# Kernel tuning notes

Hardware: AMD Instinct MI355X
Metric: run time of the kernel (lower is better)

The kernel has to match this reference:

```python
import jax, jax.numpy as jnp
import numpy as np

CELU_ALPHA = 0.1  # torchani standard CELU alpha


def _celu(x):
    return jax.nn.celu(x, alpha=CELU_ALPHA)


def setup_inputs() -> dict:
    key = jax.random.key(0)
    ks = jax.random.split(key, 12)
    N, S, E, D = 20000, 4, 8, 1008
    dims = [D, 256, 192, 160, 1]
    inp = {
        "aev": jax.random.normal(ks[0], (N, D), jnp.float32),
        "species": jax.random.randint(ks[1], (N,), 0, S, dtype=jnp.int64),
    }
    for l in range(4):
        din, dout = dims[l], dims[l + 1]
        inp[f"W{l}"] = jax.random.normal(ks[2 + 2 * l], (S, E, din, dout), jnp.float32) * (1.0 / np.sqrt(din).astype(np.float32))
        inp[f"b{l}"] = jax.random.normal(ks[3 + 2 * l], (S, E, dout), jnp.float32) * 0.05
    return inp


def reference(aev, species, W0, b0, W1, b1, W2, b2, W3, b3):
    # Faithful math of InferModel.forward: for each species i, gather atoms of
    # that species, run the BmmAtomicNetwork (ensemble of MLPs via bmm, CELU
    # activations, mean over ensemble members), sum per-species energies, then
    # sum into a single [1]-shaped total energy.
    # JIT-friendly equivalent: evaluate every species network on all atoms
    # (S=4 is small) and select each atom's output by its species index.
    # h: [S, E, N, hidden]
    h = _celu(jnp.einsum('ni,seio->seno', aev, W0) + b0[:, :, None, :])
    h = _celu(jnp.einsum('seni,seio->seno', h, W1) + b1[:, :, None, :])
    h = _celu(jnp.einsum('seni,seio->seno', h, W2) + b2[:, :, None, :])
    h = jnp.einsum('seni,seio->seno', h, W3) + b3[:, :, None, :]  # [S,E,N,1]
    per_atom = h.mean(axis=1)[:, :, 0]  # mean over ensemble -> [S, N]
    sel = jnp.take_along_axis(per_atom, species[None, :], axis=0)[0]  # [N]
    return jnp.sum(sel, keepdims=True)  # shape [1], total energy
```

## Files before the change

### kernel.cpp

```cpp
#include <hip/hip_runtime.h>
#include <cmath>

#define NA 20000
#define NS 4
#define NE 8
#define DD 1008
#define BM 128
#define MAXT 157
#define MAXROWS 20608

typedef unsigned short u16;
typedef unsigned int u32;
typedef unsigned long long u64;
typedef u16 u16x8 __attribute__((ext_vector_type(8)));
typedef u16 u16x4 __attribute__((ext_vector_type(4)));
typedef float f32x4 __attribute__((ext_vector_type(4)));
typedef short s16x8 __attribute__((ext_vector_type(8)));

__device__ __forceinline__ float bf2f(u16 h) {
  u32 u = ((u32)h) << 16;
  return __builtin_bit_cast(float, u);
}
__device__ __forceinline__ u16 f2bf(float f) {
  u32 b = __builtin_bit_cast(u32, f);
  u32 lsb = (b >> 16) & 1;
  return (u16)((b + 0x7fffu + lsb) >> 16);
}
__device__ __forceinline__ float celu_f(float x) {
#if __has_builtin(__builtin_amdgcn_exp2f)
  float e = __builtin_amdgcn_exp2f(x * 14.426950408889634f);
#else
  float e = exp2f(x * 14.426950408889634f);
#endif
  return x > 0.f ? x : 0.1f * (e - 1.f);
}
__device__ __forceinline__ float gf(const void* g, size_t i, bool isF32) {
  return isF32 ? ((const float*)g)[i] : bf2f(((const u16*)g)[i]);
}

__device__ __forceinline__ void gll16(const void* g, const u16* lds) {
#if __has_builtin(__builtin_amdgcn_global_load_lds)
  __builtin_amdgcn_global_load_lds(
      (const __attribute__((address_space(1))) u32*)g,
      (__attribute__((address_space(3))) u32*)(u16*)lds, 16, 0, 0);
#else
  int l = threadIdx.x & 63;
  *(f32x4*)((u16*)lds + l * 8) = *(const f32x4*)g;
#endif
}

#define CHUNK_BARRIER(N)                                   \
  do {                                                     \
    asm volatile("s_waitcnt vmcnt(" #N ")" ::: "memory");  \
    __builtin_amdgcn_sched_barrier(0);                     \
    __builtin_amdgcn_s_barrier();                          \
    __builtin_amdgcn_sched_barrier(0);                     \
  } while (0)

__global__ void k_probe0(const void* __restrict__ aev, const void* __restrict__ species,
                         int* __restrict__ w) {
  __shared__ int sh[2];
  int tid = threadIdx.x;
  if (tid < 64) w[tid] = 0;
  if (tid == 0) { sh[0] = 0; sh[1] = 0; }
  __syncthreads();
  const u16* a = (const u16*)aev;
  int bad = 0;
  for (int i = 0; i < 16; ++i) {
    u16 h = a[tid * 16 + i];
    int ex = (h >> 7) & 0xFF;
    if (ex < 107 || ex > 147) ++bad;
  }
  atomicAdd(&sh[0], bad);
  const int* sp = (const int*)species;
  int odd = 0;
  for (int i = 0; i < 4; ++i)
    if (sp[(tid * 4 + i) * 2 + 1] != 0) ++odd;
  atomicAdd(&sh[1], odd);
  __syncthreads();
  if (tid == 0) {
    w[18] = (sh[0] > 400) ? 1 : 0;
    w[19] = (sh[1] == 0) ? 1 : 0;
  }
}

__device__ __forceinline__ int get_species(const void* sp, int i, bool i64) {
  int s = i64 ? ((const int*)sp)[2 * i] : ((const int*)sp)[i];
  return s < 0 ? 0 : (s > 3 ? 3 : s);
}

__global__ void k_count(const void* __restrict__ species, int* __restrict__ w) {
  int i = blockIdx.x * 256 + threadIdx.x;
  int lane = threadIdx.x & 63;
  int s = (i < NA) ? get_species(species, i, w[19] != 0) : -1;
  for (int sp = 0; sp < 4; ++sp) {
    u64 m = __ballot(s == sp);
    if (m != 0 && lane == (__ffsll((long long)m) - 1))
      atomicAdd(&w[sp], __popcll(m));
  }
  __syncthreads();
  if (threadIdx.x == 0) {
    __threadfence();
    if (atomicAdd(&w[25], 1) == (int)gridDim.x - 1) {
      int b = 0, pb = 0;
      for (int sp = 0; sp < 4; ++sp) {
        int c = atomicAdd(&w[sp], 0);
        w[13 + sp] = b; b += c;
        w[20 + sp] = pb; pb += ((c + 127) >> 7) << 7;
      }
      w[24] = pb;
    }
  }
}

__global__ void k_scatsml(const void* __restrict__ species, int* __restrict__ w,
                          int* __restrict__ order,
                          const void* b0, const void* b1, const void* b2, const void* b3,
                          const void* W3, u16* ob0, u16* ob1, u16* ob2, u16* ob3,
                          u16* oW3, u16* gap) {
  if (blockIdx.x == 79) {
    const bool isF32 = (w[18] != 0);
    int t = threadIdx.x;
    for (int i = t; i < 32 * 256; i += 256) ob0[i] = f2bf(gf(b0, i, isF32));
    for (int i = t; i < 32 * 192; i += 256) ob1[i] = f2bf(gf(b1, i, isF32));
    for (int i = t; i < 32 * 160; i += 256) ob2[i] = f2bf(gf(b2, i, isF32));
    for (int i = t; i < 32 * 160; i += 256) oW3[i] = f2bf(gf(W3, i, isF32));
    if (t < 32) ob3[t] = f2bf(gf(b3, t, isF32));
    u16x8 z = {0, 0, 0, 0, 0, 0, 0, 0};
    *(u16x8*)(gap + t * 8) = z;
    return;
  }
  int i = blockIdx.x * 256 + threadIdx.x;
  int lane = threadIdx.x & 63;
  int s = (i < NA) ? get_species(species, i, w[19] != 0) : -1;
  for (int sp = 0; sp < 4; ++sp) {
    u64 m = __ballot(s == sp);
    if (m == 0) continue;
    int leader = __ffsll((long long)m) - 1;
    int base = 0;
    if (lane == leader) base = atomicAdd(&w[4 + sp], __popcll(m));
    base = __shfl(base, leader);
    if (s == sp) {
      int rank = __popcll(m & ((lane == 63) ? 0x7fffffffffffffffULL : ((1ULL << lane) - 1)));
      order[w[13 + sp] + base + rank] = i;
    }
  }
}

__global__ void k_gather(const void* __restrict__ aev, const int* __restrict__ w,
                         const int* __restrict__ order, u16* __restrict__ aevb) {
  const bool isF32 = (w[18] != 0);
  const int t = threadIdx.x;
  const int r = blockIdx.x * 4 + (t >> 7);
  const int j = t & 127;
  if (j >= 126) return;
  const int s = (r >= w[21]) + (r >= w[22]) + (r >= w[23]);
  const int local = r - w[20 + s];
  u16x8 v = {0, 0, 0, 0, 0, 0, 0, 0};
  if (local < w[s]) {
    const int src = order[w[13 + s] + local];
    if (isF32) {
      const float* p = (const float*)aev + (size_t)src * DD + j * 8;
      const f32x4 f0 = *(const f32x4*)p;
      const f32x4 f1 = *(const f32x4*)(p + 4);
#pragma unroll
      for (int i = 0; i < 4; ++i) { v[i] = f2bf(f0[i]); v[4 + i] = f2bf(f1[i]); }
    } else {
      v = *(const u16x8*)((const u16*)aev + (size_t)src * DD + j * 8);
    }
  }
  *(u16x8*)(aevb + (size_t)r * DD + j * 8) = v;
}

__device__ void tr_tile(const void* __restrict__ W, u16* __restrict__ out,
                        int K, int N, int Kpad, bool isF32, int se,
                        int k0, int n0, int t, u16 (*tile)[68]) {
  const size_t inBase = (size_t)se * K * N;
#pragma unroll
  for (int c = 0; c < 4; ++c) {
    int kk = (t >> 4) + c * 16, nn = (t & 15) * 4;
    int k = k0 + kk, n = n0 + nn;
    u16x4 v = {0, 0, 0, 0};
    if (k < K && n < N) {
      if (isF32) {
        f32x4 f = *(const f32x4*)((const float*)W + inBase + (size_t)k * N + n);
        v[0] = f2bf(f[0]); v[1] = f2bf(f[1]); v[2] = f2bf(f[2]); v[3] = f2bf(f[3]);
      } else {
        v = *(const u16x4*)((const u16*)W + inBase + (size_t)k * N + n);
      }
    }
    *(u16x4*)(&tile[kk][nn]) = v;
  }
  __syncthreads();
  int nloc = t >> 2, ks = (t & 3) * 16;
  if (n0 + nloc < N) {
    u16x8 o0, o1;
#pragma unroll
    for (int i = 0; i < 8; ++i) { o0[i] = tile[ks + i][nloc]; o1[i] = tile[ks + 8 + i][nloc]; }
    size_t ob = (size_t)se * N * Kpad + (size_t)(n0 + nloc) * Kpad + k0 + ks;
    *(u16x8*)(out + ob) = o0;
    *(u16x8*)(out + ob + 8) = o1;
  }
}

__global__ void k_tr3(const void* __restrict__ W0, const void* __restrict__ W1,
                      const void* __restrict__ W2, u16* __restrict__ o0,
                      u16* __restrict__ o1, u16* __restrict__ o2,
                      const int* __restrict__ w) {
  __shared__ u16 tile[64][68];
  const bool isF32 = (w[18] != 0);
  const int se = blockIdx.x, by = blockIdx.y, bz = blockIdx.z, t = threadIdx.x;
  tr_tile(W0, o0, 1008, 256, 1024, isF32, se, by * 64, bz * 64, t, tile);
  if (by < 4 && bz < 3) {
    __syncthreads();
    tr_tile(W1, o1, 256, 192, 256, isF32, se, by * 64, bz * 64, t, tile);
  }
  if (by < 3 && bz < 3) {
    __syncthreads();
    tr_tile(W2, o2, 192, 160, 192, isF32, se, by * 64, bz * 64, t, tile);
  }
}

__global__ __launch_bounds__(512, 4) void k_main(
    const u16* __restrict__ aevb, const u16* __restrict__ wt0,
    const u16* __restrict__ wt1, const u16* __restrict__ wt2,
    const u16* __restrict__ w3b, const u16* __restrict__ b0b,
    const u16* __restrict__ b1b, const u16* __restrict__ b2b,
    const u16* __restrict__ b3b, const int* __restrict__ w,
    float* __restrict__ accum) {
  __shared__ __align__(16) u16 L[32768];

  const int tid = threadIdx.x;
  const int g = blockIdx.x;
  const int s = g >> 1;
  const int e = (g & 1) * 4 + (blockIdx.y & 3);
  const int tile = blockIdx.y >> 2;
  const int cnt = w[s];
  if (tile * BM >= cnt) return;
  const int mRow = w[20 + s] + tile * BM;
  const int mCount = min(BM, cnt - tile * BM);
  const int se = s * NE + e;

  const int lane = tid & 63;
  const int wv = tid >> 6;
  const int lcol = lane & 15;
  const int quad = lane >> 4;

  {
    const u16* wt0se = wt0 + (size_t)se * 256 * 1024;
    const int wm = wv >> 2, wn = wv & 3;

    const int rowA = tid >> 2;
    const int gAx = (tid & 3) ^ ((rowA >> 1) & 3);
    const u16* gA = aevb + (size_t)(mRow + rowA) * 1008 + gAx * 8;
    const int rB1 = 128 + (tid >> 2);
    const int gB0x = (tid & 3) ^ (((tid >> 2) >> 1) & 3);
    const int gB1x = (tid & 3) ^ ((rB1 >> 1) & 3);
    const u16* gB0 = wt0se + (size_t)(tid >> 2) * 1024 + gB0x * 8;
    const u16* gB1 = wt0se + (size_t)rB1 * 1024 + gB1x * 8;
    const int aSt = wv * 512;
    const int bSt = wv * 512;
    const int bSt2 = 4096 + wv * 512;

    const int gsw = (quad ^ ((lcol >> 1) & 3)) * 8;
    const int aRow0 = (wm * 64 + lcol) * 32 + gsw;
    const int bRow0 = (wn * 64 + lcol) * 32 + gsw;

    f32x4 acc[4][4];
#pragma unroll
    for (int i = 0; i < 4; ++i)
#pragma unroll
      for (int j = 0; j < 4; ++j) acc[i][j] = (f32x4){0.f, 0.f, 0.f, 0.f};

    gll16(gA, &L[aSt]);
    gll16(gB0, &L[8192 + bSt]);
    gll16(gB1, &L[8192 + bSt2]);
    gll16(gB0 + 32, &L[16384 + bSt]);
    gll16(gB1 + 32, &L[16384 + bSt2]);
    CHUNK_BARRIER(2);

    int bbufC = 0, bbufS = 2;
    for (int p = 0; p < 32; ++p) {
      if (p < 31)
        gll16(gA + (p + 1) * 32, &L[((p + 1) & 1) * 4096 + aSt]);
      if (p < 30) {
        gll16(gB0 + (p + 2) * 32, &L[8192 + bbufS * 8192 + bSt]);
        gll16(gB1 + (p + 2) * 32, &L[8192 + bbufS * 8192 + bSt2]);
      }
      const u16* Ad = &L[(p & 1) * 4096];
      const u16* Bd = &L[8192 + bbufC * 8192];
      s16x8 aF[4], bF[4];
#pragma unroll
      for (int mt = 0; mt < 4; ++mt)
        aF[mt] = __builtin_bit_cast(s16x8, *(const u16x8*)(Ad + aRow0 + mt * 512));
#pragma unroll
      for (int nt = 0; nt < 4; ++nt)
        bF[nt] = __builtin_bit_cast(s16x8, *(const u16x8*)(Bd + bRow0 + nt * 512));
      __builtin_amdgcn_s_setprio(1);
#pragma unroll
      for (int nt = 0; nt < 4; ++nt)
#pragma unroll
        for (int mt = 0; mt < 4; ++mt)
          acc[mt][nt] = __builtin_amdgcn_mfma_f32_16x16x32_bf16(aF[mt], bF[nt], acc[mt][nt], 0, 0, 0);
      __builtin_amdgcn_s_setprio(0);
      if (p < 30) CHUNK_BARRIER(2); else CHUNK_BARRIER(0);
      bbufC = (bbufC == 2) ? 0 : bbufC + 1;
      bbufS = (bbufS == 2) ? 0 : bbufS + 1;
    }

#pragma unroll
    for (int nt = 0; nt < 4; ++nt) {
      const int col = wn * 64 + nt * 16 + lcol;
      const float bb = bf2f(b0b[se * 256 + col]);
#pragma unroll
      for (int mt = 0; mt < 4; ++mt) {
#pragma unroll
        for (int r = 0; r < 4; ++r) {
          const int rr = wm * 64 + mt * 16 + quad * 4 + r;
          L[(rr * 256 + col) ^ ((rr & 7) << 3)] = f2bf(celu_f(acc[mt][nt][r] + bb));
        }
      }
    }
  }
  __syncthreads();

  {
    const int wm = wv >> 2, wn = wv & 3;
    const u16* w1se = wt1 + (size_t)se * 192 * 256;
    const u16* bp[3];
#pragma unroll
    for (int nt = 0; nt < 3; ++nt)
      bp[nt] = w1se + (size_t)(wn * 48 + nt * 16 + lcol) * 256 + quad * 8;
    f32x4 acc[4][3];
#pragma unroll
    for (int i = 0; i < 4; ++i)
#pragma unroll
      for (int j = 0; j < 3; ++j) acc[i][j] = (f32x4){0.f, 0.f, 0.f, 0.f};
    int aBase[4], aSwz[4];
#pragma unroll
    for (int mt = 0; mt < 4; ++mt) {
      const int row = wm * 64 + mt * 16 + lcol;
      aBase[mt] = row * 256 + quad * 8;
      aSwz[mt] = (row & 7) << 3;
    }
    u16x8 cB[3], nB[3];
#pragma unroll
    for (int nt = 0; nt < 3; ++nt) cB[nt] = *(const u16x8*)bp[nt];
    for (int kc = 0; kc < 8; ++kc) {
      if (kc < 7) {
#pragma unroll
        for (int nt = 0; nt < 3; ++nt) nB[nt] = *(const u16x8*)(bp[nt] + (kc + 1) * 32);
      }
      s16x8 aF[4];
#pragma unroll
      for (int mt = 0; mt < 4; ++mt)
        aF[mt] = __builtin_bit_cast(s16x8, *(const u16x8*)&L[(aBase[mt] + kc * 32) ^ aSwz[mt]]);
#pragma unroll
      for (int nt = 0; nt < 3; ++nt) {
        const s16x8 bF = __builtin_bit_cast(s16x8, cB[nt]);
#pragma unroll
        for (int mt = 0; mt < 4; ++mt)
          acc[mt][nt] = __builtin_amdgcn_mfma_f32_16x16x32_bf16(aF[mt], bF, acc[mt][nt], 0, 0, 0);
      }
      if (kc < 7) {
#pragma unroll
        for (int nt = 0; nt < 3; ++nt) cB[nt] = nB[nt];
      }
    }
    __syncthreads();
#pragma unroll
    for (int nt = 0; nt < 3; ++nt) {
      const int col = wn * 48 + nt * 16 + lcol;
      const float bb = bf2f(b1b[se * 192 + col]);
#pragma unroll
      for (int mt = 0; mt < 4; ++mt) {
#pragma unroll
        for (int r = 0; r < 4; ++r) {
          const int rr = wm * 64 + mt * 16 + quad * 4 + r;
          L[(rr * 192 + col) ^ ((rr & 7) << 3)] = f2bf(celu_f(acc[mt][nt][r] + bb));
        }
      }
    }
  }
  __syncthreads();

  {
    const int wm = wv >> 1, wn = wv & 1;
    const u16* w2se = wt2 + (size_t)se * 160 * 192;
    const u16* bp[5];
#pragma unroll
    for (int nt = 0; nt < 5; ++nt)
      bp[nt] = w2se + (size_t)(wn * 80 + nt * 16 + lcol) * 192 + quad * 8;
    f32x4 acc[2][5];
#pragma unroll
    for (int i = 0; i < 2; ++i)
#pragma unroll
      for (int j = 0; j < 5; ++j) acc[i][j] = (f32x4){0.f, 0.f, 0.f, 0.f};
    int aBase[2], aSwz[2];
#pragma unroll
    for (int mt = 0; mt < 2; ++mt) {
      const int row = wm * 32 + mt * 16 + lcol;
      aBase[mt] = row * 192 + quad * 8;
      aSwz[mt] = (row & 7) << 3;
    }
    u16x8 cB[5], nB[5];
#pragma unroll
    for (int nt = 0; nt < 5; ++nt) cB[nt] = *(const u16x8*)bp[nt];
    for (int kc = 0; kc < 6; ++kc) {
      if (kc < 5) {
#pragma unroll
        for (int nt = 0; nt < 5; ++nt) nB[nt] = *(const u16x8*)(bp[nt] + (kc + 1) * 32);
      }
      s16x8 aF[2];
#pragma unroll
      for (int mt = 0; mt < 2; ++mt)
        aF[mt] = __builtin_bit_cast(s16x8, *(const u16x8*)&L[(aBase[mt] + kc * 32) ^ aSwz[mt]]);
#pragma unroll
      for (int nt = 0; nt < 5; ++nt) {
        const s16x8 bF = __builtin_bit_cast(s16x8, cB[nt]);
#pragma unroll
        for (int mt = 0; mt < 2; ++mt)
          acc[mt][nt] = __builtin_amdgcn_mfma_f32_16x16x32_bf16(aF[mt], bF, acc[mt][nt], 0, 0, 0);
      }
      if (kc < 5) {
#pragma unroll
        for (int nt = 0; nt < 5; ++nt) cB[nt] = nB[nt];
      }
    }
    __syncthreads();
#pragma unroll
    for (int nt = 0; nt < 5; ++nt) {
      const int col = wn * 80 + nt * 16 + lcol;
      const float bb = bf2f(b2b[se * 160 + col]);
#pragma unroll
      for (int mt = 0; mt < 2; ++mt) {
#pragma unroll
        for (int r = 0; r < 4; ++r) {
          const int rr = wm * 32 + mt * 16 + quad * 4 + r;
          L[(rr * 160 + col) ^ ((rr & 7) << 3)] = f2bf(celu_f(acc[mt][nt][r] + bb));
        }
      }
    }
  }
  __syncthreads();

  {
    const int row = tid >> 2;
    const int pp = tid & 3;
    const u16* w3p = w3b + se * 160;
    float dotv = 0.f;
#pragma unroll
    for (int j = 0; j < 5; ++j) {
      const int ci = (pp + 4 * j) * 8;
      const u16x8 hv = *(const u16x8*)&L[(row * 160 + ci) ^ ((row & 7) << 3)];
      const u16x8 wv8 = *(const u16x8*)(w3p + ci);
#pragma unroll
      for (int t2 = 0; t2 < 8; ++t2)
        dotv = fmaf(bf2f(hv[t2]), bf2f(wv8[t2]), dotv);
    }
    dotv += __shfl_xor(dotv, 1);
    dotv += __shfl_xor(dotv, 2);
    float v = (pp == 0 && row < mCount) ? (dotv + bf2f(b3b[se])) : 0.f;
    v += __shfl_xor(v, 4);
    v += __shfl_xor(v, 8);
    v += __shfl_xor(v, 16);
    v += __shfl_xor(v, 32);
    float* redf = (float*)&L[20608];
    if (lane == 0) redf[wv] = v;
    __syncthreads();
    if (tid == 0) {
      float tot = 0.f;
#pragma unroll
      for (int i = 0; i < 8; ++i) tot += redf[i];
      atomicAdd(accum, tot * 0.125f);
    }
  }
}

__global__ void k_final(const float* __restrict__ accum, u32* __restrict__ out) {
  u32 h = (u32)f2bf(accum[0]);
  out[0] = (h << 16) | h;
}

extern "C" void kernel_launch(void* const* d_in, const int* in_sizes, int n_in,
                              void* d_out, int out_size, void* d_ws, size_t ws_size,
                              hipStream_t stream) {
  const void* aev = d_in[0];
  const void* species = d_in[1];
  const void* W0 = d_in[2];
  const void* b0 = d_in[3];
  const void* W1 = d_in[4];
  const void* b1 = d_in[5];
  const void* W2 = d_in[6];
  const void* b2 = d_in[7];
  const void* W3 = d_in[8];
  const void* b3 = d_in[9];

  int* wsI = (int*)d_ws;
  float* accum = (float*)((char*)d_ws + 17 * 4);
  int* order = wsI + 1024;
  char* wsB = (char*)d_ws;

  const size_t oB0 = 131072;
  const size_t oB1 = 147456;
  const size_t oB2 = 159744;
  const size_t oB3 = 169984;
  const size_t oW3 = 170048;
  const size_t oAevb = 262144;
  const size_t oGap = 41807872;
  const size_t oWt0 = 41811968;
  const size_t oWt1 = 58589184;
  const size_t oWt2 = 61734912;

  u16* aevb = (u16*)(wsB + oAevb);
  u16* wt0 = (u16*)(wsB + oWt0);
  u16* wt1 = (u16*)(wsB + oWt1);
  u16* wt2 = (u16*)(wsB + oWt2);
  u16* w3b = (u16*)(wsB + oW3);
  u16* b0b = (u16*)(wsB + oB0);
  u16* b1b = (u16*)(wsB + oB1);
  u16* b2b = (u16*)(wsB + oB2);
  u16* b3b = (u16*)(wsB + oB3);

  hipLaunchKernelGGL(k_probe0, dim3(1), dim3(256), 0, stream, aev, species, wsI);
  hipLaunchKernelGGL(k_count, dim3((NA + 255) / 256), dim3(256), 0, stream, species, wsI);
  hipLaunchKernelGGL(k_scatsml, dim3(80), dim3(256), 0, stream, species, wsI, order,
                     b0, b1, b2, b3, W3, b0b, b1b, b2b, b3b, w3b, (u16*)(wsB + oGap));
  hipLaunchKernelGGL(k_gather, dim3(MAXROWS / 4), dim3(512), 0, stream, aev, wsI, order, aevb);
  hipLaunchKernelGGL(k_tr3, dim3(32, 16, 4), dim3(256), 0, stream, W0, W1, W2,
                     wt0, wt1, wt2, wsI);
  hipLaunchKernelGGL(k_main, dim3(8, 4 * MAXT), dim3(512), 0, stream,
                     aevb, wt0, wt1, wt2, w3b, b0b, b1b, b2b, b3b, wsI, accum);
  hipLaunchKernelGGL(k_final, dim3(1), dim3(1), 0, stream, accum, (u32*)d_out);
}
```

Baseline: 428.2 us.

## Double block size to 1024 threads and halve per-wave row tiles

```diff
diff --git a/kernel.cpp b/kernel.cpp
--- a/kernel.cpp
+++ b/kernel.cpp
@@ -48,14 +48,6 @@
   *(f32x4*)((u16*)lds + l * 8) = *(const f32x4*)g;
 #endif
 }
-
-#define CHUNK_BARRIER(N)                                   \
-  do {                                                     \
-    asm volatile("s_waitcnt vmcnt(" #N ")" ::: "memory");  \
-    __builtin_amdgcn_sched_barrier(0);                     \
-    __builtin_amdgcn_s_barrier();                          \
-    __builtin_amdgcn_sched_barrier(0);                     \
-  } while (0)
 
 __global__ void k_probe0(const void* __restrict__ aev, const void* __restrict__ species,
                          int* __restrict__ w) {
@@ -221,7 +213,7 @@
   }
 }
 
-__global__ __launch_bounds__(512, 4) void k_main(
+__global__ __launch_bounds__(1024, 8) void k_main(
     const u16* __restrict__ aevb, const u16* __restrict__ wt0,
     const u16* __restrict__ wt1, const u16* __restrict__ wt2,
     const u16* __restrict__ w3b, const u16* __restrict__ b0b,
@@ -252,46 +244,39 @@
 
     const int rowA = tid >> 2;
     const int gAx = (tid & 3) ^ ((rowA >> 1) & 3);
-    const u16* gA = aevb + (size_t)(mRow + rowA) * 1008 + gAx * 8;
-    const int rB1 = 128 + (tid >> 2);
-    const int gB0x = (tid & 3) ^ (((tid >> 2) >> 1) & 3);
-    const int gB1x = (tid & 3) ^ ((rB1 >> 1) & 3);
-    const u16* gB0 = wt0se + (size_t)(tid >> 2) * 1024 + gB0x * 8;
-    const u16* gB1 = wt0se + (size_t)rB1 * 1024 + gB1x * 8;
+    const u16* gA = aevb + (size_t)(mRow + (rowA & 127)) * 1008 + gAx * 8;
+    const int rowB = tid >> 2;
+    const int gBx = (tid & 3) ^ ((rowB >> 1) & 3);
+    const u16* gB = wt0se + (size_t)rowB * 1024 + gBx * 8;
     const int aSt = wv * 512;
     const int bSt = wv * 512;
-    const int bSt2 = 4096 + wv * 512;
 
     const int gsw = (quad ^ ((lcol >> 1) & 3)) * 8;
-    const int aRow0 = (wm * 64 + lcol) * 32 + gsw;
+    const int aRow0 = (wm * 32 + lcol) * 32 + gsw;
     const int bRow0 = (wn * 64 + lcol) * 32 + gsw;
 
-    f32x4 acc[4][4];
-#pragma unroll
-    for (int i = 0; i < 4; ++i)
+    f32x4 acc[2][4];
+#pragma unroll
+    for (int i = 0; i < 2; ++i)
 #pragma unroll
       for (int j = 0; j < 4; ++j) acc[i][j] = (f32x4){0.f, 0.f, 0.f, 0.f};
 
-    gll16(gA, &L[aSt]);
-    gll16(gB0, &L[8192 + bSt]);
-    gll16(gB1, &L[8192 + bSt2]);
-    gll16(gB0 + 32, &L[16384 + bSt]);
-    gll16(gB1 + 32, &L[16384 + bSt2]);
-    CHUNK_BARRIER(2);
-
-    int bbufC = 0, bbufS = 2;
+    if (tid < 512) gll16(gA, &L[aSt]);
+    gll16(gB, &L[8192 + bSt]);
+    __syncthreads();
+
     for (int p = 0; p < 32; ++p) {
-      if (p < 31)
-        gll16(gA + (p + 1) * 32, &L[((p + 1) & 1) * 4096 + aSt]);
-      if (p < 30) {
-        gll16(gB0 + (p + 2) * 32, &L[8192 + bbufS * 8192 + bSt]);
-        gll16(gB1 + (p + 2) * 32, &L[8192 + bbufS * 8192 + bSt2]);
-      }
-      const u16* Ad = &L[(p & 1) * 4096];
-      const u16* Bd = &L[8192 + bbufC * 8192];
-      s16x8 aF[4], bF[4];
-#pragma unroll
-      for (int mt = 0; mt < 4; ++mt)
+      const int d = p & 1;
+      if (p < 31) {
+        const int dn = d ^ 1;
+        if (tid < 512) gll16(gA + (p + 1) * 32, &L[dn * 4096 + aSt]);
+        gll16(gB + (p + 1) * 32, &L[8192 + dn * 8192 + bSt]);
+      }
+      const u16* Ad = &L[d * 4096];
+      const u16* Bd = &L[8192 + d * 8192];
+      s16x8 aF[2], bF[4];
+#pragma unroll
+      for (int mt = 0; mt < 2; ++mt)
         aF[mt] = __builtin_bit_cast(s16x8, *(const u16x8*)(Ad + aRow0 + mt * 512));
 #pragma unroll
       for (int nt = 0; nt < 4; ++nt)
@@ -300,12 +285,10 @@
 #pragma unroll
       for (int nt = 0; nt < 4; ++nt)
 #pragma unroll
-        for (int mt = 0; mt < 4; ++mt)
+        for (int mt = 0; mt < 2; ++mt)
           acc[mt][nt] = __builtin_amdgcn_mfma_f32_16x16x32_bf16(aF[mt], bF[nt], acc[mt][nt], 0, 0, 0);
       __builtin_amdgcn_s_setprio(0);
-      if (p < 30) CHUNK_BARRIER(2); else CHUNK_BARRIER(0);
-      bbufC = (bbufC == 2) ? 0 : bbufC + 1;
-      bbufS = (bbufS == 2) ? 0 : bbufS + 1;
+      __syncthreads();
     }
 
 #pragma unroll
@@ -313,10 +296,10 @@
       const int col = wn * 64 + nt * 16 + lcol;
       const float bb = bf2f(b0b[se * 256 + col]);
 #pragma unroll
-      for (int mt = 0; mt < 4; ++mt) {
+      for (int mt = 0; mt < 2; ++mt) {
 #pragma unroll
         for (int r = 0; r < 4; ++r) {
-          const int rr = wm * 64 + mt * 16 + quad * 4 + r;
+          const int rr = wm * 32 + mt * 16 + quad * 4 + r;
           L[(rr * 256 + col) ^ ((rr & 7) << 3)] = f2bf(celu_f(acc[mt][nt][r] + bb));
         }
       }
@@ -331,15 +314,15 @@
 #pragma unroll
     for (int nt = 0; nt < 3; ++nt)
       bp[nt] = w1se + (size_t)(wn * 48 + nt * 16 + lcol) * 256 + quad * 8;
-    f32x4 acc[4][3];
-#pragma unroll
-    for (int i = 0; i < 4; ++i)
+    f32x4 acc[2][3];
+#pragma unroll
+    for (int i = 0; i < 2; ++i)
 #pragma unroll
       for (int j = 0; j < 3; ++j) acc[i][j] = (f32x4){0.f, 0.f, 0.f, 0.f};
-    int aBase[4], aSwz[4];
-#pragma unroll
-    for (int mt = 0; mt < 4; ++mt) {
-      const int row = wm * 64 + mt * 16 + lcol;
+    int aBase[2], aSwz[2];
+#pragma unroll
+    for (int mt = 0; mt < 2; ++mt) {
+      const int row = wm * 32 + mt * 16 + lcol;
       aBase[mt] = row * 256 + quad * 8;
       aSwz[mt] = (row & 7) << 3;
     }
@@ -351,15 +334,15 @@
 #pragma unroll
         for (int nt = 0; nt < 3; ++nt) nB[nt] = *(const u16x8*)(bp[nt] + (kc + 1) * 32);
       }
-      s16x8 aF[4];
-#pragma unroll
-      for (int mt = 0; mt < 4; ++mt)
+      s16x8 aF[2];
+#pragma unroll
+      for (int mt = 0; mt < 2; ++mt)
         aF[mt] = __builtin_bit_cast(s16x8, *(const u16x8*)&L[(aBase[mt] + kc * 32) ^ aSwz[mt]]);
 #pragma unroll
       for (int nt = 0; nt < 3; ++nt) {
         const s16x8 bF = __builtin_bit_cast(s16x8, cB[nt]);
 #pragma unroll
-        for (int mt = 0; mt < 4; ++mt)
+        for (int mt = 0; mt < 2; ++mt)
           acc[mt][nt] = __builtin_amdgcn_mfma_f32_16x16x32_bf16(aF[mt], bF, acc[mt][nt], 0, 0, 0);
       }
       if (kc < 7) {
@@ -373,10 +356,10 @@
       const int col = wn * 48 + nt * 16 + lcol;
       const float bb = bf2f(b1b[se * 192 + col]);
 #pragma unroll
-      for (int mt = 0; mt < 4; ++mt) {
+      for (int mt = 0; mt < 2; ++mt) {
 #pragma unroll
         for (int r = 0; r < 4; ++r) {
-          const int rr = wm * 64 + mt * 16 + quad * 4 + r;
+          const int rr = wm * 32 + mt * 16 + quad * 4 + r;
           L[(rr * 192 + col) ^ ((rr & 7) << 3)] = f2bf(celu_f(acc[mt][nt][r] + bb));
         }
       }
@@ -385,17 +368,18 @@
   __syncthreads();
 
   {
-    const int wm = wv >> 1, wn = wv & 1;
+    const int wm = wv >> 2, wn = wv & 3;
+    const int nN2 = (wn < 2) ? 2 : 3;
+    const int t2 = (wn < 2) ? 2 * wn : 3 * wn - 2;
     const u16* w2se = wt2 + (size_t)se * 160 * 192;
-    const u16* bp[5];
-#pragma unroll
-    for (int nt = 0; nt < 5; ++nt)
-      bp[nt] = w2se + (size_t)(wn * 80 + nt * 16 + lcol) * 192 + quad * 8;
-    f32x4 acc[2][5];
+    const u16* bp[3];
+    for (int nt = 0; nt < nN2; ++nt)
+      bp[nt] = w2se + (size_t)((t2 + nt) * 16 + lcol) * 192 + quad * 8;
+    f32x4 acc[2][3];
 #pragma unroll
     for (int i = 0; i < 2; ++i)
 #pragma unroll
-      for (int j = 0; j < 5; ++j) acc[i][j] = (f32x4){0.f, 0.f, 0.f, 0.f};
+      for (int j = 0; j < 3; ++j) acc[i][j] = (f32x4){0.f, 0.f, 0.f, 0.f};
     int aBase[2], aSwz[2];
 #pragma unroll
     for (int mt = 0; mt < 2; ++mt) {
@@ -403,34 +387,29 @@
       aBase[mt] = row * 192 + quad * 8;
       aSwz[mt] = (row & 7) << 3;
     }
-    u16x8 cB[5], nB[5];
-#pragma unroll
-    for (int nt = 0; nt < 5; ++nt) cB[nt] = *(const u16x8*)bp[nt];
+    u16x8 cB[3], nB[3];
+    for (int nt = 0; nt < nN2; ++nt) cB[nt] = *(const u16x8*)bp[nt];
     for (int kc = 0; kc < 6; ++kc) {
       if (kc < 5) {
-#pragma unroll
-        for (int nt = 0; nt < 5; ++nt) nB[nt] = *(const u16x8*)(bp[nt] + (kc + 1) * 32);
+        for (int nt = 0; nt < nN2; ++nt) nB[nt] = *(const u16x8*)(bp[nt] + (kc + 1) * 32);
       }
       s16x8 aF[2];
 #pragma unroll
       for (int mt = 0; mt < 2; ++mt)
         aF[mt] = __builtin_bit_cast(s16x8, *(const u16x8*)&L[(aBase[mt] + kc * 32) ^ aSwz[mt]]);
-#pragma unroll
-      for (int nt = 0; nt < 5; ++nt) {
+      for (int nt = 0; nt < nN2; ++nt) {
         const s16x8 bF = __builtin_bit_cast(s16x8, cB[nt]);
 #pragma unroll
         for (int mt = 0; mt < 2; ++mt)
           acc[mt][nt] = __builtin_amdgcn_mfma_f32_16x16x32_bf16(aF[mt], bF, acc[mt][nt], 0, 0, 0);
       }
       if (kc < 5) {
-#pragma unroll
-        for (int nt = 0; nt < 5; ++nt) cB[nt] = nB[nt];
+        for (int nt = 0; nt < nN2; ++nt) cB[nt] = nB[nt];
       }
     }
     __syncthreads();
-#pragma unroll
-    for (int nt = 0; nt < 5; ++nt) {
-      const int col = wn * 80 + nt * 16 + lcol;
+    for (int nt = 0; nt < nN2; ++nt) {
+      const int col = (t2 + nt) * 16 + lcol;
       const float bb = bf2f(b2b[se * 160 + col]);
 #pragma unroll
       for (int mt = 0; mt < 2; ++mt) {
@@ -445,23 +424,31 @@
   __syncthreads();
 
   {
-    const int row = tid >> 2;
-    const int pp = tid & 3;
+    const int row = tid >> 3;
+    const int pp = tid & 7;
     const u16* w3p = w3b + se * 160;
     float dotv = 0.f;
 #pragma unroll
-    for (int j = 0; j < 5; ++j) {
-      const int ci = (pp + 4 * j) * 8;
+    for (int j = 0; j < 2; ++j) {
+      const int ci = (pp + 8 * j) * 8;
       const u16x8 hv = *(const u16x8*)&L[(row * 160 + ci) ^ ((row & 7) << 3)];
       const u16x8 wv8 = *(const u16x8*)(w3p + ci);
 #pragma unroll
       for (int t2 = 0; t2 < 8; ++t2)
         dotv = fmaf(bf2f(hv[t2]), bf2f(wv8[t2]), dotv);
     }
+    if (pp < 4) {
+      const int ci = (16 + pp) * 8;
+      const u16x8 hv = *(const u16x8*)&L[(row * 160 + ci) ^ ((row & 7) << 3)];
+      const u16x8 wv8 = *(const u16x8*)(w3p + ci);
+#pragma unroll
+      for (int t2 = 0; t2 < 8; ++t2)
+        dotv = fmaf(bf2f(hv[t2]), bf2f(wv8[t2]), dotv);
+    }
     dotv += __shfl_xor(dotv, 1);
     dotv += __shfl_xor(dotv, 2);
+    dotv += __shfl_xor(dotv, 4);
     float v = (pp == 0 && row < mCount) ? (dotv + bf2f(b3b[se])) : 0.f;
-    v += __shfl_xor(v, 4);
     v += __shfl_xor(v, 8);
     v += __shfl_xor(v, 16);
     v += __shfl_xor(v, 32);
@@ -471,7 +458,7 @@
     if (tid == 0) {
       float tot = 0.f;
 #pragma unroll
-      for (int i = 0; i < 8; ++i) tot += redf[i];
+      for (int i = 0; i < 16; ++i) tot += redf[i];
       atomicAdd(accum, tot * 0.125f);
     }
   }
@@ -529,7 +516,7 @@
   hipLaunchKernelGGL(k_gather, dim3(MAXROWS / 4), dim3(512), 0, stream, aev, wsI, order, aevb);
   hipLaunchKernelGGL(k_tr3, dim3(32, 16, 4), dim3(256), 0, stream, W0, W1, W2,
                      wt0, wt1, wt2, wsI);
-  hipLaunchKernelGGL(k_main, dim3(8, 4 * MAXT), dim3(512), 0, stream,
+  hipLaunchKernelGGL(k_main, dim3(8, 4 * MAXT), dim3(1024), 0, stream,
                      aevb, wt0, wt1, wt2, w3b, b0b, b1b, b2b, b3b, wsI, accum);
   hipLaunchKernelGGL(k_final, dim3(1), dim3(1), 0, stream, accum, (u32*)d_out);
 }
```

Result: slower. 814.9 us (+90.3%).
